# Optimization experiments

Hardware: AMD Instinct MI355X
Metric: run time of the kernel (lower is better)

## Reference

```python
import jax, jax.numpy as jnp
import numpy as np

B, Q, H, KVH, HD, HS = 2, 1024, 32, 8, 64, 2048
LCK = 2  # number of pre-existing cache entries
N_REP = H // KVH


def setup_inputs() -> dict:
    key = jax.random.key(0)
    ks = jax.random.split(key, 8)
    s = 0.02
    causal = jnp.tril(jnp.ones((Q, Q), dtype=bool))
    attention_mask = jnp.where(causal, 0.0, -1e9).astype(jnp.float32)[None, None]  # [1,1,Q,Q]
    return {
        "hidden_states": jax.random.normal(ks[0], (B, Q, 2 * HS), jnp.float32),
        "Wq": jax.random.normal(ks[1], (H * HD, 2 * HS), jnp.float32) * s,
        "Wk": jax.random.normal(ks[2], (KVH * HD, 2 * HS), jnp.float32) * s,
        "Wv": jax.random.normal(ks[3], (KVH * HD, 2 * HS), jnp.float32) * s,
        "Wo": jax.random.normal(ks[4], (H * HD, HS), jnp.float32).T * s,  # [HS, H*HD]
        "cache_k": jax.random.normal(ks[5], (LCK, B, H, Q, HD), jnp.float32),
        "cache_v": jax.random.normal(ks[6], (LCK, B, H, Q, HD), jnp.float32),
        "attention_mask": attention_mask,
        "position_ids": jnp.broadcast_to(jnp.arange(Q, dtype=jnp.int32), (B, Q)),
    }


def _rotate_half(x):
    return jnp.concatenate([-x[..., HD // 2:], x[..., :HD // 2]], axis=-1)


def reference(hidden_states, Wq, Wk, Wv, Wo, cache_k, cache_v, attention_mask, position_ids):
    b, q_len, _ = hidden_states.shape
    # QKV projections (Linear with weight [out,in]: x @ W.T)
    q = (hidden_states @ Wq.T).reshape(b, q_len, H, HD).transpose(0, 2, 1, 3)    # [b,H,q,hd]
    k = (hidden_states @ Wk.T).reshape(b, q_len, KVH, HD).transpose(0, 2, 1, 3)  # [b,KVH,q,hd]
    v = (hidden_states @ Wv.T).reshape(b, q_len, KVH, HD).transpose(0, 2, 1, 3)

    # RoPE at positions position_ids + lck (lck = LCK cached entries)
    inv_freq = 1.0 / (10000.0 ** (jnp.arange(0, HD, 2, dtype=jnp.float32) / HD))
    pos = (position_ids + LCK).astype(jnp.float32)                 # [b,q]
    freqs = pos[..., None] * inv_freq                              # [b,q,hd/2]
    emb = jnp.concatenate([freqs, freqs], axis=-1)                 # [b,q,hd]
    cos = jnp.cos(emb)[:, None]                                    # [b,1,q,hd]
    sin = jnp.sin(emb)[:, None]
    q = q * cos + _rotate_half(q) * sin
    k = k * cos + _rotate_half(k) * sin

    # GQA repeat_kv
    k = jnp.repeat(k, N_REP, axis=1)  # [b,H,q,hd]
    v = jnp.repeat(v, N_REP, axis=1)

    scale = 1.0 / np.sqrt(HD)
    k0, v0 = cache_k[0], cache_v[0]
    # full attention against first cache entry (+ causal mask)
    w0 = jnp.einsum('bhqd,bhkd->bhqk', q, k0) * scale + attention_mask  # [b,H,q,q]
    # per-step diagonal attention against remaining cache entries + fresh k
    tail_k = jnp.concatenate([cache_k[1:], k[None]], axis=0)  # [LCK,b,H,q,hd]
    tail_v = jnp.concatenate([cache_v[1:], v[None]], axis=0)
    wtail = jnp.einsum('bhqd,nbhqd->bhqn', q, tail_k) * scale  # [b,H,q,LCK]

    w = jnp.concatenate([w0, wtail], axis=-1)
    w = jax.nn.softmax(w.astype(jnp.float32), axis=-1).astype(q.dtype)

    out = jnp.einsum('bhqk,bhkd->bhqd', w[..., :q_len], v0)
    out = out + jnp.einsum('bhqn,nbhqd->bhqd', w[..., q_len:], tail_v)

    out = out.transpose(0, 2, 1, 3).reshape(b, q_len, H * HD)
    return out @ Wo.T  # [b,q,HS]
```

## Files before the change

kernel.cpp:

```cpp
#include <hip/hip_runtime.h>
#include <hip/hip_bf16.h>
#include <math.h>

#define B_    2
#define Q_    1024
#define H_    32
#define KVH_  8
#define HD_   64
#define HS_   2048
#define NREP_ 4
#define KIN_  (2*HS_)
#define M_    (B_*Q_)
#define QKVN_ (H_*HD_ + 2*KVH_*HD_)
#define AOW_  (H_*HD_)
#define SCALE_ 0.125f

typedef __attribute__((ext_vector_type(8))) short bf16x8;
typedef __attribute__((ext_vector_type(4))) float f32x4;
typedef unsigned short u16;

static __device__ __forceinline__ u16 f2b(float f) {
  union { float f; unsigned int u; } c; c.f = f;
  unsigned int r = (c.u + 0x7fffu + ((c.u >> 16) & 1u)) >> 16;
  return (u16)r;
}
static __device__ __forceinline__ float b2f(u16 s) {
  union { unsigned int u; float f; } c;
  c.u = ((unsigned int)s) << 16;
  return c.f;
}
static __device__ __forceinline__ unsigned long long pack4s(float4 v, float sc) {
  return (unsigned long long)f2b(v.x*sc) |
         ((unsigned long long)f2b(v.y*sc) << 16) |
         ((unsigned long long)f2b(v.z*sc) << 32) |
         ((unsigned long long)f2b(v.w*sc) << 48);
}

#define GLOAD(SRC, DST) __builtin_amdgcn_global_load_lds( \
    (const __attribute__((address_space(1))) void*)(SRC), \
    (__attribute__((address_space(3))) void*)(DST), 16, 0, 0)

__global__ __launch_bounds__(256) void cast_f32_bf16(
    const float* __restrict__ src, u16* __restrict__ dst, long n)
{
  long i = ((long)blockIdx.x * blockDim.x + threadIdx.x) * 8;
  if (i >= n) return;
  float4 a = *(const float4*)(src + i);
  float4 b = *(const float4*)(src + i + 4);
  unsigned long long o[2] = {pack4s(a, 1.f), pack4s(b, 1.f)};
  *(float4*)(dst + i) = *(const float4*)o;
}

__global__ __launch_bounds__(256) void cast_kv(
    const float* __restrict__ k0, const float* __restrict__ v0,
    u16* __restrict__ Kb, u16* __restrict__ Vtb)
{
  __shared__ float Vs[64][65];
  const int kt = blockIdx.x, bh = blockIdx.y;
  const int t = threadIdx.x;
  const int r = t >> 2, seg = t & 3;

  {
    const float* sp = k0 + ((size_t)bh*Q_ + (kt<<6) + r)*64;
    u16* dp = Kb + ((size_t)bh*Q_ + (kt<<6) + r)*64;
#pragma unroll
    for (int c2 = 2*seg; c2 < 2*seg+2; ++c2) {
      int ca = c2 ^ (r & 7);
      float4 a = *(const float4*)(sp + ca*8);
      float4 b = *(const float4*)(sp + ca*8 + 4);
      unsigned long long o[2] = {pack4s(a,1.f), pack4s(b,1.f)};
      *(float4*)(dp + c2*8) = *(const float4*)o;
    }
  }
  {
    const float* sp = v0 + ((size_t)bh*Q_ + (kt<<6) + r)*64 + seg*16;
#pragma unroll
    for (int c = 0; c < 4; ++c) {
      float4 v = *(const float4*)(sp + 4*c);
      Vs[r][seg*16 + 4*c + 0] = v.x; Vs[r][seg*16 + 4*c + 1] = v.y;
      Vs[r][seg*16 + 4*c + 2] = v.z; Vs[r][seg*16 + 4*c + 3] = v.w;
    }
  }
  __syncthreads();
  {
    const int d = r;
    u16* dp = Vtb + ((size_t)bh*64 + d)*Q_ + (kt<<6);
#pragma unroll
    for (int c2 = 2*seg; c2 < 2*seg+2; ++c2) {
      int ca = c2 ^ (d & 7);
      u16 o[8];
#pragma unroll
      for (int j = 0; j < 8; ++j) o[j] = f2b(Vs[ca*8 + j][d]);
      *(float4*)(dp + c2*8) = *(const float4*)o;
    }
  }
}

template<bool OUT_BF16>
__global__ __launch_bounds__(256, 3) void gemm_nt(
    const u16* __restrict__ A, const u16* __restrict__ W,
    void* __restrict__ Cv, int K, int ldc)
{
  __shared__ u16 As[2*128*64];
  __shared__ u16 Bs[2*64*64];
  const int m0 = blockIdx.y << 7, n0 = blockIdx.x << 6;
  const int t = threadIdx.x;
  const int wave = t >> 6, lane = t & 63;
  const int wr = wave >> 1, wc = wave & 1;

  f32x4 acc[4][2] = {};

  const int lrow8 = lane >> 3;
  const int lcsw  = ((lane & 7) ^ lrow8) * 8;
  const int fr    = lane & 15;
  const int g     = lane >> 4;

#define GEMM_STAGE(BUF, K0) do { \
    _Pragma("unroll") \
    for (int p = 0; p < 4; ++p) { \
      int rbase = p * 32 + wave * 8; \
      GLOAD(A + (size_t)(m0 + rbase + lrow8) * K + (K0) + lcsw, \
            As + (BUF)*8192 + rbase * 64); \
    } \
    _Pragma("unroll") \
    for (int p = 0; p < 2; ++p) { \
      int rbase = p * 32 + wave * 8; \
      GLOAD(W + (size_t)(n0 + rbase + lrow8) * K + (K0) + lcsw, \
            Bs + (BUF)*4096 + rbase * 64); \
    } \
  } while(0)

  GEMM_STAGE(0, 0);
  int cur = 0;
  for (int k0 = 0; k0 < K; k0 += 64) {
    if (k0 + 64 < K) {
      GEMM_STAGE(cur ^ 1, k0 + 64);
      asm volatile("s_waitcnt vmcnt(6)" ::: "memory");
    } else {
      asm volatile("s_waitcnt vmcnt(0)" ::: "memory");
    }
    asm volatile("s_barrier" ::: "memory");

    const u16* Ab = As + cur*8192;
    const u16* Bb = Bs + cur*4096;
    bf16x8 af[4][2], bfr[2][2];
#pragma unroll
    for (int kk = 0; kk < 2; ++kk) {
      int ck = kk * 4 + g;
#pragma unroll
      for (int mi = 0; mi < 4; ++mi) {
        int row = wr * 64 + mi * 16 + fr;
        af[mi][kk] = *(const bf16x8*)(Ab + row * 64 + ((ck ^ (row & 7)) << 3));
      }
#pragma unroll
      for (int ni = 0; ni < 2; ++ni) {
        int row = wc * 32 + ni * 16 + fr;
        bfr[ni][kk] = *(const bf16x8*)(Bb + row * 64 + ((ck ^ (row & 7)) << 3));
      }
    }
    __builtin_amdgcn_s_setprio(1);
#pragma unroll
    for (int kk = 0; kk < 2; ++kk)
#pragma unroll
      for (int mi = 0; mi < 4; ++mi)
#pragma unroll
        for (int ni = 0; ni < 2; ++ni)
          acc[mi][ni] = __builtin_amdgcn_mfma_f32_16x16x32_bf16(af[mi][kk], bfr[ni][kk], acc[mi][ni], 0, 0, 0);
    __builtin_amdgcn_s_setprio(0);
    asm volatile("s_barrier" ::: "memory");
    cur ^= 1;
  }
#undef GEMM_STAGE

#pragma unroll
  for (int mi = 0; mi < 4; ++mi) {
    int rbase = m0 + wr * 64 + mi * 16 + (lane >> 4) * 4;
#pragma unroll
    for (int ni = 0; ni < 2; ++ni) {
      int col = n0 + wc * 32 + ni * 16 + (lane & 15);
#pragma unroll
      for (int r = 0; r < 4; ++r) {
        if (OUT_BF16) ((u16*)Cv)[(size_t)(rbase + r) * ldc + col] = f2b(acc[mi][ni][r]);
        else          ((float*)Cv)[(size_t)(rbase + r) * ldc + col] = acc[mi][ni][r];
      }
    }
  }
}

__global__ void rope_kernel(u16* __restrict__ Yb, const int* __restrict__ pos_ids)
{
  int idx = blockIdx.x * blockDim.x + threadIdx.x;
  const int nwork = M_ * 40 * 4;
  if (idx >= nwork) return;
  int dblk = idx & 3;
  int hr   = idx >> 2;
  int head = hr % 40;
  int m    = hr / 40;
  u16* row = Yb + (size_t)m * QKVN_ + head * 64;
  int d0 = dblk * 8;
  float4 lo4 = *(const float4*)(row + d0);
  float4 hi4 = *(const float4*)(row + d0 + 32);
  const u16* lo = (const u16*)&lo4;
  const u16* hi = (const u16*)&hi4;
  float p = (float)(pos_ids[m] + 2);
  float qs = (head < 32) ? SCALE_ : 1.0f;
  u16 olo[8], ohi[8];
#pragma unroll
  for (int i = 0; i < 8; ++i) {
    int d = d0 + i;
    float inv = exp2f(-0.4152410118609203f * (float)d);
    float f = p * inv;
    float c, s;
    sincosf(f, &s, &c);
    float x0 = b2f(lo[i]), x1 = b2f(hi[i]);
    olo[i] = f2b((x0*c - x1*s) * qs);
    ohi[i] = f2b((x1*c + x0*s) * qs);
  }
  *(float4*)(row + d0)      = *(const float4*)olo;
  *(float4*)(row + d0 + 32) = *(const float4*)ohi;
}

__global__ __launch_bounds__(256, 3) void attn_mfma(
    const u16* __restrict__ Yb,
    const u16* __restrict__ Kb,
    const u16* __restrict__ Vtb,
    const float* __restrict__ cache_k,
    const float* __restrict__ cache_v,
    u16* __restrict__ AOb)
{
  __shared__ u16 Qs[64*64];
  __shared__ u16 Ps[64*64];
  __shared__ u16 Ks[2*64*64];
  __shared__ u16 Vt[2*64*64];

  const int bid = blockIdx.x;
  const int xcd = bid & 7, within = bid >> 3;
  const int w16 = within & 15;
  const int qt = (w16 & 1) ? (15 - (w16 >> 1)) : (w16 >> 1);
  const int pair = xcd * 8 + (within >> 4);
  const int h = pair >> 1, b = pair & 1;
  const int bh = b * H_ + h;

  const int t = threadIdx.x;
  const int wave = t >> 6, lane = t & 63;
  const int g = lane >> 4, sub = lane & 15;
  const int wq0 = wave * 16;
  const int srow = (lane >> 3);
  const int scc  = lane & 7;

  const u16* KbT = Kb + (size_t)bh * Q_ * 64;
  const u16* VtT = Vtb + (size_t)bh * 64 * Q_;

#define ATTN_STAGE(BUF, KT) do { \
    _Pragma("unroll") \
    for (int p = 0; p < 2; ++p) { \
      int r = p*32 + wave*8 + srow; \
      GLOAD(KbT + (size_t)(((KT)<<6) + r)*64 + scc*8, Ks + (BUF)*4096 + p*2048 + wave*512); \
      GLOAD(VtT + (size_t)r*Q_ + ((KT)<<6) + scc*8,   Vt + (BUF)*4096 + p*2048 + wave*512); \
    } \
  } while(0)

  {
#pragma unroll
    for (int p = 0; p < 2; ++p) {
      int r = p*32 + wave*8 + srow;
      GLOAD(Yb + (size_t)(b*Q_ + (qt<<6) + r)*QKVN_ + h*64 + ((scc ^ (r&7))<<3),
            Qs + p*2048 + wave*512);
    }
  }
  ATTN_STAGE(0, 0);
  asm volatile("s_waitcnt vmcnt(4)" ::: "memory");
  asm volatile("s_barrier" ::: "memory");

  bf16x8 qb[2];
#pragma unroll
  for (int kk = 0; kk < 2; ++kk) {
    int row = wq0 + sub;
    qb[kk] = *(const bf16x8*)&Qs[row*64 + (((4*kk+g) ^ (row&7))<<3)];
  }

  float m_run = -3e38f, l_run = 0.f;
  f32x4 acc_o[4] = {};
  int cur = 0;

  for (int kt = 0; kt <= qt; ++kt) {
    if (kt < qt) {
      ATTN_STAGE(cur ^ 1, kt + 1);
      asm volatile("s_waitcnt vmcnt(4)" ::: "memory");
    } else {
      asm volatile("s_waitcnt vmcnt(0)" ::: "memory");
    }
    asm volatile("s_barrier" ::: "memory");

    const u16* ksb = Ks + cur*4096;
    const u16* vtb = Vt + cur*4096;

    f32x4 s[4] = {};
    __builtin_amdgcn_s_setprio(1);
#pragma unroll
    for (int kk = 0; kk < 2; ++kk) {
      int kb = 4*kk + g;
#pragma unroll
      for (int cb = 0; cb < 4; ++cb) {
        int krow = cb*16 + sub;
        bf16x8 kf = *(const bf16x8*)&ksb[krow*64 + ((kb ^ (krow&7))<<3)];
        s[cb] = __builtin_amdgcn_mfma_f32_16x16x32_bf16(kf, qb[kk], s[cb], 0, 0, 0);
      }
    }
    __builtin_amdgcn_s_setprio(0);

    if (kt == qt) {
#pragma unroll
      for (int cb = 0; cb < 4; ++cb)
#pragma unroll
        for (int r = 0; r < 4; ++r)
          if (cb*16 + 4*g + r > wq0 + sub) s[cb][r] = -3e38f;
    }

    float mt = -3e38f;
#pragma unroll
    for (int cb = 0; cb < 4; ++cb)
#pragma unroll
      for (int r = 0; r < 4; ++r) mt = fmaxf(mt, s[cb][r]);
    mt = fmaxf(mt, __shfl_xor(mt, 16, 64));
    mt = fmaxf(mt, __shfl_xor(mt, 32, 64));

    float al = 1.0f;
    if (__any(mt > m_run + 8.f)) {
      float mnew = fmaxf(m_run, mt);
      al = __expf(m_run - mnew);
      m_run = mnew;
      int base = (lane & 48) + ((lane & 48) >> 2);
#pragma unroll
      for (int r = 0; r < 4; ++r) {
        float alr = __shfl(al, base + r, 64);
#pragma unroll
        for (int db = 0; db < 4; ++db) acc_o[db][r] *= alr;
      }
    }

    float sum = 0.f;
#pragma unroll
    for (int cb = 0; cb < 4; ++cb) {
      float p0 = __expf(s[cb][0]-m_run), p1 = __expf(s[cb][1]-m_run);
      float p2 = __expf(s[cb][2]-m_run), p3 = __expf(s[cb][3]-m_run);
      sum += (p0+p1)+(p2+p3);
      unsigned long long pk =
          (unsigned long long)((unsigned int)f2b(p0) | ((unsigned int)f2b(p1)<<16)) |
          ((unsigned long long)((unsigned int)f2b(p2) | ((unsigned int)f2b(p3)<<16)) << 32);
      int col8 = cb*2 + (g>>1);
      int dst = (wq0 + sub)*64 + ((col8 ^ (sub&7))<<3) + ((g&1)<<2);
      *(unsigned long long*)&Ps[dst] = pk;
    }
    sum += __shfl_xor(sum, 16, 64);
    sum += __shfl_xor(sum, 32, 64);
    l_run = l_run*al + sum;

    __builtin_amdgcn_s_setprio(1);
#pragma unroll
    for (int kk = 0; kk < 2; ++kk) {
      bf16x8 pa = *(const bf16x8*)&Ps[(wq0 + sub)*64 + (((4*kk+g) ^ (sub&7))<<3)];
#pragma unroll
      for (int db = 0; db < 4; ++db) {
        int drow = db*16 + sub;
        bf16x8 vf = *(const bf16x8*)&vtb[drow*64 + (((4*kk+g) ^ (drow&7))<<3)];
        acc_o[db] = __builtin_amdgcn_mfma_f32_16x16x32_bf16(pa, vf, acc_o[db], 0, 0, 0);
      }
    }
    __builtin_amdgcn_s_setprio(0);
    asm volatile("s_barrier" ::: "memory");
    cur ^= 1;
  }
#undef ATTN_STAGE

  const int qrow_mine = wq0 + sub;
  const int qpos_mine = (qt<<6) + qrow_mine;
  float e1 = 0.f, e2 = 0.f;
  {
    const float* k1p = cache_k + ((size_t)((B_ + b)*H_ + h)*Q_ + qpos_mine)*HD_ + g*16;
    const u16*   kfp = Yb + (size_t)(b*Q_ + qpos_mine)*QKVN_ + H_*HD_ + (h/NREP_)*HD_ + g*16;
    float qv[16];
#pragma unroll
    for (int half = 0; half < 2; ++half) {
      int kb = 2*g + half;
      bf16x8 qq = *(const bf16x8*)&Qs[qrow_mine*64 + ((kb ^ (qrow_mine&7))<<3)];
#pragma unroll
      for (int i = 0; i < 8; ++i) qv[half*8 + i] = b2f(((u16)qq[i]));
    }
    float4 kf4a = *(const float4*)kfp;
    float4 kf4b = *(const float4*)(kfp + 8);
    const u16* kf16a = (const u16*)&kf4a;
    const u16* kf16b = (const u16*)&kf4b;
#pragma unroll
    for (int c = 0; c < 4; ++c) {
      float4 kv1 = *(const float4*)(k1p + 4*c);
      e1 += qv[4*c]*kv1.x + qv[4*c+1]*kv1.y + qv[4*c+2]*kv1.z + qv[4*c+3]*kv1.w;
    }
#pragma unroll
    for (int i = 0; i < 8; ++i) {
      e2 += qv[i]   * b2f(kf16a[i]);
      e2 += qv[8+i] * b2f(kf16b[i]);
    }
  }
  e1 += __shfl_xor(e1, 16, 64); e1 += __shfl_xor(e1, 32, 64);
  e2 += __shfl_xor(e2, 16, 64); e2 += __shfl_xor(e2, 32, 64);

#pragma unroll
  for (int r = 0; r < 4; ++r) {
    int row = 4*g + r;
    int src = (lane & 48) | row;
    float e1r = __shfl(e1, src, 64);
    float e2r = __shfl(e2, src, 64);
    float m_r = __shfl(m_run, src, 64);
    float l_r = __shfl(l_run, src, 64);
    float mnew = fmaxf(m_r, fmaxf(e1r, e2r));
    float alr = __expf(m_r - mnew);
    float w1  = __expf(e1r - mnew);
    float w2  = __expf(e2r - mnew);
    float linv = 1.f / (l_r*alr + w1 + w2);
    int qpos = (qt<<6) + wq0 + row;
    const float* v1p = cache_v + ((size_t)((B_ + b)*H_ + h)*Q_ + qpos)*HD_;
    const u16*   vfp = Yb + (size_t)(b*Q_ + qpos)*QKVN_ + (H_*HD_ + KVH_*HD_) + (h/NREP_)*HD_;
    u16* op = AOb + (size_t)(b*Q_ + qpos)*AOW_ + h*HD_;
#pragma unroll
    for (int db = 0; db < 4; ++db) {
      int d = db*16 + sub;
      float o = (acc_o[db][r]*alr + w1*v1p[d] + w2*b2f(vfp[d])) * linv;
      op[d] = f2b(o);
    }
  }
}

extern "C" void kernel_launch(void* const* d_in, const int* in_sizes, int n_in,
                              void* d_out, int out_size, void* d_ws, size_t ws_size,
                              hipStream_t stream) {
  const float* hidden  = (const float*)d_in[0];
  const float* Wq      = (const float*)d_in[1];
  const float* Wk      = (const float*)d_in[2];
  const float* Wv      = (const float*)d_in[3];
  const float* Wo      = (const float*)d_in[4];
  const float* cache_k = (const float*)d_in[5];
  const float* cache_v = (const float*)d_in[6];
  const int*   pos_ids = (const int*)d_in[8];
  float* out = (float*)d_out;

  char* ws = (char*)d_ws;
  u16* Yb  = (u16*)ws;  ws += (size_t)M_ * QKVN_ * 2;
  u16* Xb  = (u16*)ws;  ws += (size_t)M_ * KIN_ * 2;
  u16* Wb  = (u16*)ws;  ws += (size_t)QKVN_ * KIN_ * 2;
  u16* Wob = (u16*)ws;  ws += (size_t)HS_ * AOW_ * 2;
  u16* Kb  = (u16*)ws;  ws += (size_t)B_*H_*Q_*64 * 2;
  u16* Vtb = (u16*)ws;  ws += (size_t)B_*H_*Q_*64 * 2;
  u16* AOb = Xb;

  {
    long n;
    n = (long)M_ * KIN_;
    cast_f32_bf16<<<dim3((n/8 + 255)/256), 256, 0, stream>>>(hidden, Xb, n);
    n = (long)H_*HD_*KIN_;
    cast_f32_bf16<<<dim3((n/8 + 255)/256), 256, 0, stream>>>(Wq, Wb, n);
    n = (long)KVH_*HD_*KIN_;
    cast_f32_bf16<<<dim3((n/8 + 255)/256), 256, 0, stream>>>(Wk, Wb + (size_t)2048*KIN_, n);
    cast_f32_bf16<<<dim3((n/8 + 255)/256), 256, 0, stream>>>(Wv, Wb + (size_t)2560*KIN_, n);
    n = (long)HS_ * AOW_;
    cast_f32_bf16<<<dim3((n/8 + 255)/256), 256, 0, stream>>>(Wo, Wob, n);
  }
  cast_kv<<<dim3(16, 64), 256, 0, stream>>>(cache_k, cache_v, Kb, Vtb);

  gemm_nt<true><<<dim3(QKVN_/64, M_/128), 256, 0, stream>>>(Xb, Wb, (void*)Yb, KIN_, QKVN_);
  rope_kernel<<<dim3((M_*40*4 + 255)/256), 256, 0, stream>>>(Yb, pos_ids);
  attn_mfma<<<dim3(1024), 256, 0, stream>>>(Yb, Kb, Vtb, cache_k, cache_v, AOb);
  gemm_nt<false><<<dim3(HS_/64, M_/128), 256, 0, stream>>>(AOb, Wob, (void*)out, AOW_, HS_);
}
```

Before: 180.7 us.

## Fuse casts into one kernel, fold RoPE into QKV GEMM, widen attention blocks

The five weight and activation cast launches are merged into a single grid-stride kernel. RoPE and the Q scaling move into the QKV GEMM epilogue, with partner halves exchanged through shared memory, so the separate rope pass over Yb goes away. Attention blocks grow to 512 threads covering 128 query rows that share each K/V tile load, and per-wave causal skipping is added. This trades launch overhead and repeated K/V traffic for higher register and LDS pressure per block and extra syncs in the GEMM epilogue.

```diff
diff --git a/kernel.cpp b/kernel.cpp
--- a/kernel.cpp
+++ b/kernel.cpp
@@ -40,15 +40,29 @@
     (const __attribute__((address_space(1))) void*)(SRC), \
     (__attribute__((address_space(3))) void*)(DST), 16, 0, 0)
 
-__global__ __launch_bounds__(256) void cast_f32_bf16(
-    const float* __restrict__ src, u16* __restrict__ dst, long n)
+__global__ __launch_bounds__(256) void cast_all(
+    const float* __restrict__ hidden, const float* __restrict__ Wq,
+    const float* __restrict__ Wk, const float* __restrict__ Wv,
+    const float* __restrict__ Wo,
+    u16* __restrict__ Xb, u16* __restrict__ Wb, u16* __restrict__ Wob)
 {
-  long i = ((long)blockIdx.x * blockDim.x + threadIdx.x) * 8;
-  if (i >= n) return;
-  float4 a = *(const float4*)(src + i);
-  float4 b = *(const float4*)(src + i + 4);
-  unsigned long long o[2] = {pack4s(a, 1.f), pack4s(b, 1.f)};
-  *(float4*)(dst + i) = *(const float4*)o;
+  const int U0 = 1048576;
+  const int U1 = U0 + 1048576;
+  const int U2 = U1 + 262144;
+  const int U3 = U2 + 262144;
+  const int U4 = U3 + 524288;
+  for (int u = blockIdx.x*blockDim.x + threadIdx.x; u < U4; u += gridDim.x*blockDim.x) {
+    const float* src; u16* dst;
+    if (u < U0)      { src = hidden + (size_t)u*8;   dst = Xb + (size_t)u*8; }
+    else if (u < U1) { src = Wq + (size_t)(u-U0)*8;  dst = Wb + (size_t)(u-U0)*8; }
+    else if (u < U2) { src = Wk + (size_t)(u-U1)*8;  dst = Wb + (size_t)2048*KIN_ + (size_t)(u-U1)*8; }
+    else if (u < U3) { src = Wv + (size_t)(u-U2)*8;  dst = Wb + (size_t)2560*KIN_ + (size_t)(u-U2)*8; }
+    else             { src = Wo + (size_t)(u-U3)*8;  dst = Wob + (size_t)(u-U3)*8; }
+    float4 a = *(const float4*)src;
+    float4 bb = *(const float4*)(src + 4);
+    unsigned long long o[2] = {pack4s(a, 1.f), pack4s(bb, 1.f)};
+    *(float4*)dst = *(const float4*)o;
+  }
 }
 
 __global__ __launch_bounds__(256) void cast_kv(
@@ -59,7 +73,6 @@
   const int kt = blockIdx.x, bh = blockIdx.y;
   const int t = threadIdx.x;
   const int r = t >> 2, seg = t & 3;
-
   {
     const float* sp = k0 + ((size_t)bh*Q_ + (kt<<6) + r)*64;
     u16* dp = Kb + ((size_t)bh*Q_ + (kt<<6) + r)*64;
@@ -96,10 +109,10 @@
   }
 }
 
-template<bool OUT_BF16>
+template<bool QKV>
 __global__ __launch_bounds__(256, 3) void gemm_nt(
     const u16* __restrict__ A, const u16* __restrict__ W,
-    void* __restrict__ Cv, int K, int ldc)
+    void* __restrict__ Cv, int K, int ldc, const int* __restrict__ pos_ids)
 {
   __shared__ u16 As[2*128*64];
   __shared__ u16 Bs[2*64*64];
@@ -172,55 +185,59 @@
   }
 #undef GEMM_STAGE
 
-#pragma unroll
-  for (int mi = 0; mi < 4; ++mi) {
-    int rbase = m0 + wr * 64 + mi * 16 + (lane >> 4) * 4;
-#pragma unroll
-    for (int ni = 0; ni < 2; ++ni) {
-      int col = n0 + wc * 32 + ni * 16 + (lane & 15);
+  if (QKV && n0 < 2560) {
+    float* xch = (float*)As;
+    __syncthreads();
+#pragma unroll
+    for (int mi = 0; mi < 4; ++mi)
+#pragma unroll
+      for (int ni = 0; ni < 2; ++ni)
+#pragma unroll
+        for (int r = 0; r < 4; ++r)
+          xch[(wr*64 + mi*16 + g*4 + r)*64 + wc*32 + ni*16 + (lane & 15)] = acc[mi][ni][r];
+    __syncthreads();
+    const bool isq = (n0 < 2048);
+    u16* outp = (u16*)Cv;
+#pragma unroll
+    for (int mi = 0; mi < 4; ++mi) {
 #pragma unroll
       for (int r = 0; r < 4; ++r) {
-        if (OUT_BF16) ((u16*)Cv)[(size_t)(rbase + r) * ldc + col] = f2b(acc[mi][ni][r]);
-        else          ((float*)Cv)[(size_t)(rbase + r) * ldc + col] = acc[mi][ni][r];
-      }
-    }
-  }
-}
-
-__global__ void rope_kernel(u16* __restrict__ Yb, const int* __restrict__ pos_ids)
-{
-  int idx = blockIdx.x * blockDim.x + threadIdx.x;
-  const int nwork = M_ * 40 * 4;
-  if (idx >= nwork) return;
-  int dblk = idx & 3;
-  int hr   = idx >> 2;
-  int head = hr % 40;
-  int m    = hr / 40;
-  u16* row = Yb + (size_t)m * QKVN_ + head * 64;
-  int d0 = dblk * 8;
-  float4 lo4 = *(const float4*)(row + d0);
-  float4 hi4 = *(const float4*)(row + d0 + 32);
-  const u16* lo = (const u16*)&lo4;
-  const u16* hi = (const u16*)&hi4;
-  float p = (float)(pos_ids[m] + 2);
-  float qs = (head < 32) ? SCALE_ : 1.0f;
-  u16 olo[8], ohi[8];
-#pragma unroll
-  for (int i = 0; i < 8; ++i) {
-    int d = d0 + i;
-    float inv = exp2f(-0.4152410118609203f * (float)d);
-    float f = p * inv;
-    float c, s;
-    sincosf(f, &s, &c);
-    float x0 = b2f(lo[i]), x1 = b2f(hi[i]);
-    olo[i] = f2b((x0*c - x1*s) * qs);
-    ohi[i] = f2b((x1*c + x0*s) * qs);
-  }
-  *(float4*)(row + d0)      = *(const float4*)olo;
-  *(float4*)(row + d0 + 32) = *(const float4*)ohi;
-}
-
-__global__ __launch_bounds__(256, 3) void attn_mfma(
+        int rl = wr*64 + mi*16 + g*4 + r;
+        int m = m0 + rl;
+        float p = (float)(pos_ids[m] + 2);
+#pragma unroll
+        for (int ni = 0; ni < 2; ++ni) {
+          int dr = ni*16 + (lane & 15);
+          float inv = exp2f(-0.4152410118609203f * (float)dr);
+          float f = p * inv;
+          float c, s;
+          sincosf(f, &s, &c);
+          float mine = acc[mi][ni][r];
+          float part = xch[rl*64 + ((wc^1)*32 + ni*16 + (lane & 15))];
+          float outv = (wc == 0) ? (mine*c - part*s) : (mine*c + part*s);
+          if (isq) outv *= SCALE_;
+          outp[(size_t)m * ldc + n0 + wc*32 + ni*16 + (lane & 15)] = f2b(outv);
+        }
+      }
+    }
+  } else {
+#pragma unroll
+    for (int mi = 0; mi < 4; ++mi) {
+      int rbase = m0 + wr * 64 + mi * 16 + g * 4;
+#pragma unroll
+      for (int ni = 0; ni < 2; ++ni) {
+        int col = n0 + wc * 32 + ni * 16 + (lane & 15);
+#pragma unroll
+        for (int r = 0; r < 4; ++r) {
+          if (QKV) ((u16*)Cv)[(size_t)(rbase + r) * ldc + col] = f2b(acc[mi][ni][r]);
+          else     ((float*)Cv)[(size_t)(rbase + r) * ldc + col] = acc[mi][ni][r];
+        }
+      }
+    }
+  }
+}
+
+__global__ __launch_bounds__(512, 4) void attn_mfma(
     const u16* __restrict__ Yb,
     const u16* __restrict__ Kb,
     const u16* __restrict__ Vtb,
@@ -228,16 +245,16 @@
     const float* __restrict__ cache_v,
     u16* __restrict__ AOb)
 {
-  __shared__ u16 Qs[64*64];
-  __shared__ u16 Ps[64*64];
+  __shared__ u16 Qs[128*64];
+  __shared__ u16 Ps[128*64];
   __shared__ u16 Ks[2*64*64];
   __shared__ u16 Vt[2*64*64];
 
   const int bid = blockIdx.x;
   const int xcd = bid & 7, within = bid >> 3;
-  const int w16 = within & 15;
-  const int qt = (w16 & 1) ? (15 - (w16 >> 1)) : (w16 >> 1);
-  const int pair = xcd * 8 + (within >> 4);
+  const int w8 = within & 7;
+  const int qtb = (w8 & 1) ? (7 - (w8 >> 1)) : (w8 >> 1);
+  const int pair = xcd * 8 + (within >> 3);
   const int h = pair >> 1, b = pair & 1;
   const int bh = b * H_ + h;
 
@@ -245,31 +262,28 @@
   const int wave = t >> 6, lane = t & 63;
   const int g = lane >> 4, sub = lane & 15;
   const int wq0 = wave * 16;
-  const int srow = (lane >> 3);
+  const int srow = lane >> 3;
   const int scc  = lane & 7;
 
   const u16* KbT = Kb + (size_t)bh * Q_ * 64;
   const u16* VtT = Vtb + (size_t)bh * 64 * Q_;
 
 #define ATTN_STAGE(BUF, KT) do { \
-    _Pragma("unroll") \
-    for (int p = 0; p < 2; ++p) { \
-      int r = p*32 + wave*8 + srow; \
-      GLOAD(KbT + (size_t)(((KT)<<6) + r)*64 + scc*8, Ks + (BUF)*4096 + p*2048 + wave*512); \
-      GLOAD(VtT + (size_t)r*Q_ + ((KT)<<6) + scc*8,   Vt + (BUF)*4096 + p*2048 + wave*512); \
-    } \
+    int r_ = wave*8 + srow; \
+    GLOAD(KbT + (size_t)(((KT)<<6) + r_)*64 + scc*8, Ks + (BUF)*4096 + wave*512); \
+    GLOAD(VtT + (size_t)r_*Q_ + ((KT)<<6) + scc*8,   Vt + (BUF)*4096 + wave*512); \
   } while(0)
 
   {
 #pragma unroll
     for (int p = 0; p < 2; ++p) {
-      int r = p*32 + wave*8 + srow;
-      GLOAD(Yb + (size_t)(b*Q_ + (qt<<6) + r)*QKVN_ + h*64 + ((scc ^ (r&7))<<3),
-            Qs + p*2048 + wave*512);
+      int r = p*64 + wave*8 + srow;
+      GLOAD(Yb + (size_t)(b*Q_ + qtb*128 + r)*QKVN_ + h*64 + ((scc ^ (r&7))<<3),
+            Qs + p*4096 + wave*512);
     }
   }
   ATTN_STAGE(0, 0);
-  asm volatile("s_waitcnt vmcnt(4)" ::: "memory");
+  asm volatile("s_waitcnt vmcnt(2)" ::: "memory");
   asm volatile("s_barrier" ::: "memory");
 
   bf16x8 qb[2];
@@ -282,99 +296,102 @@
   float m_run = -3e38f, l_run = 0.f;
   f32x4 acc_o[4] = {};
   int cur = 0;
-
-  for (int kt = 0; kt <= qt; ++kt) {
-    if (kt < qt) {
+  const int nkt = 2*qtb + 2;
+
+  for (int kt = 0; kt < nkt; ++kt) {
+    if (kt + 1 < nkt) {
       ATTN_STAGE(cur ^ 1, kt + 1);
-      asm volatile("s_waitcnt vmcnt(4)" ::: "memory");
+      asm volatile("s_waitcnt vmcnt(2)" ::: "memory");
     } else {
       asm volatile("s_waitcnt vmcnt(0)" ::: "memory");
     }
     asm volatile("s_barrier" ::: "memory");
 
-    const u16* ksb = Ks + cur*4096;
-    const u16* vtb = Vt + cur*4096;
-
-    f32x4 s[4] = {};
-    __builtin_amdgcn_s_setprio(1);
-#pragma unroll
-    for (int kk = 0; kk < 2; ++kk) {
-      int kb = 4*kk + g;
+    if (kt*64 <= qtb*128 + wq0 + 15) {
+      const u16* ksb = Ks + cur*4096;
+      const u16* vtb = Vt + cur*4096;
+
+      f32x4 s[4] = {};
+      __builtin_amdgcn_s_setprio(1);
+#pragma unroll
+      for (int kk = 0; kk < 2; ++kk) {
+        int kb = 4*kk + g;
+#pragma unroll
+        for (int cb = 0; cb < 4; ++cb) {
+          int krow = cb*16 + sub;
+          bf16x8 kf = *(const bf16x8*)&ksb[krow*64 + ((kb ^ (krow&7))<<3)];
+          s[cb] = __builtin_amdgcn_mfma_f32_16x16x32_bf16(kf, qb[kk], s[cb], 0, 0, 0);
+        }
+      }
+      __builtin_amdgcn_s_setprio(0);
+
+      if (kt >= 2*qtb) {
+#pragma unroll
+        for (int cb = 0; cb < 4; ++cb)
+#pragma unroll
+          for (int r = 0; r < 4; ++r)
+            if (kt*64 + cb*16 + 4*g + r > qtb*128 + wq0 + sub) s[cb][r] = -3e38f;
+      }
+
+      float mt = -3e38f;
+#pragma unroll
+      for (int cb = 0; cb < 4; ++cb)
+#pragma unroll
+        for (int r = 0; r < 4; ++r) mt = fmaxf(mt, s[cb][r]);
+      mt = fmaxf(mt, __shfl_xor(mt, 16, 64));
+      mt = fmaxf(mt, __shfl_xor(mt, 32, 64));
+
+      float al = 1.0f;
+      if (__any(mt > m_run + 8.f)) {
+        float mnew = fmaxf(m_run, mt);
+        al = __expf(m_run - mnew);
+        m_run = mnew;
+        int base = (lane & 48) + ((lane & 48) >> 2);
+#pragma unroll
+        for (int r = 0; r < 4; ++r) {
+          float alr = __shfl(al, base + r, 64);
+#pragma unroll
+          for (int db = 0; db < 4; ++db) acc_o[db][r] *= alr;
+        }
+      }
+
+      float sum = 0.f;
 #pragma unroll
       for (int cb = 0; cb < 4; ++cb) {
-        int krow = cb*16 + sub;
-        bf16x8 kf = *(const bf16x8*)&ksb[krow*64 + ((kb ^ (krow&7))<<3)];
-        s[cb] = __builtin_amdgcn_mfma_f32_16x16x32_bf16(kf, qb[kk], s[cb], 0, 0, 0);
-      }
-    }
-    __builtin_amdgcn_s_setprio(0);
-
-    if (kt == qt) {
-#pragma unroll
-      for (int cb = 0; cb < 4; ++cb)
-#pragma unroll
-        for (int r = 0; r < 4; ++r)
-          if (cb*16 + 4*g + r > wq0 + sub) s[cb][r] = -3e38f;
-    }
-
-    float mt = -3e38f;
-#pragma unroll
-    for (int cb = 0; cb < 4; ++cb)
-#pragma unroll
-      for (int r = 0; r < 4; ++r) mt = fmaxf(mt, s[cb][r]);
-    mt = fmaxf(mt, __shfl_xor(mt, 16, 64));
-    mt = fmaxf(mt, __shfl_xor(mt, 32, 64));
-
-    float al = 1.0f;
-    if (__any(mt > m_run + 8.f)) {
-      float mnew = fmaxf(m_run, mt);
-      al = __expf(m_run - mnew);
-      m_run = mnew;
-      int base = (lane & 48) + ((lane & 48) >> 2);
-#pragma unroll
-      for (int r = 0; r < 4; ++r) {
-        float alr = __shfl(al, base + r, 64);
-#pragma unroll
-        for (int db = 0; db < 4; ++db) acc_o[db][r] *= alr;
-      }
-    }
-
-    float sum = 0.f;
-#pragma unroll
-    for (int cb = 0; cb < 4; ++cb) {
-      float p0 = __expf(s[cb][0]-m_run), p1 = __expf(s[cb][1]-m_run);
-      float p2 = __expf(s[cb][2]-m_run), p3 = __expf(s[cb][3]-m_run);
-      sum += (p0+p1)+(p2+p3);
-      unsigned long long pk =
-          (unsigned long long)((unsigned int)f2b(p0) | ((unsigned int)f2b(p1)<<16)) |
-          ((unsigned long long)((unsigned int)f2b(p2) | ((unsigned int)f2b(p3)<<16)) << 32);
-      int col8 = cb*2 + (g>>1);
-      int dst = (wq0 + sub)*64 + ((col8 ^ (sub&7))<<3) + ((g&1)<<2);
-      *(unsigned long long*)&Ps[dst] = pk;
-    }
-    sum += __shfl_xor(sum, 16, 64);
-    sum += __shfl_xor(sum, 32, 64);
-    l_run = l_run*al + sum;
-
-    __builtin_amdgcn_s_setprio(1);
-#pragma unroll
-    for (int kk = 0; kk < 2; ++kk) {
-      bf16x8 pa = *(const bf16x8*)&Ps[(wq0 + sub)*64 + (((4*kk+g) ^ (sub&7))<<3)];
-#pragma unroll
-      for (int db = 0; db < 4; ++db) {
-        int drow = db*16 + sub;
-        bf16x8 vf = *(const bf16x8*)&vtb[drow*64 + (((4*kk+g) ^ (drow&7))<<3)];
-        acc_o[db] = __builtin_amdgcn_mfma_f32_16x16x32_bf16(pa, vf, acc_o[db], 0, 0, 0);
-      }
-    }
-    __builtin_amdgcn_s_setprio(0);
+        float p0 = __expf(s[cb][0]-m_run), p1 = __expf(s[cb][1]-m_run);
+        float p2 = __expf(s[cb][2]-m_run), p3 = __expf(s[cb][3]-m_run);
+        sum += (p0+p1)+(p2+p3);
+        unsigned long long pk =
+            (unsigned long long)((unsigned int)f2b(p0) | ((unsigned int)f2b(p1)<<16)) |
+            ((unsigned long long)((unsigned int)f2b(p2) | ((unsigned int)f2b(p3)<<16)) << 32);
+        int col8 = cb*2 + (g>>1);
+        int dst = (wq0 + sub)*64 + ((col8 ^ (sub&7))<<3) + ((g&1)<<2);
+        *(unsigned long long*)&Ps[dst] = pk;
+      }
+      sum += __shfl_xor(sum, 16, 64);
+      sum += __shfl_xor(sum, 32, 64);
+      l_run = l_run*al + sum;
+
+      __builtin_amdgcn_s_setprio(1);
+#pragma unroll
+      for (int kk = 0; kk < 2; ++kk) {
+        bf16x8 pa = *(const bf16x8*)&Ps[(wq0 + sub)*64 + (((4*kk+g) ^ (sub&7))<<3)];
+#pragma unroll
+        for (int db = 0; db < 4; ++db) {
+          int drow = db*16 + sub;
+          bf16x8 vf = *(const bf16x8*)&vtb[drow*64 + (((4*kk+g) ^ (drow&7))<<3)];
+          acc_o[db] = __builtin_amdgcn_mfma_f32_16x16x32_bf16(pa, vf, acc_o[db], 0, 0, 0);
+        }
+      }
+      __builtin_amdgcn_s_setprio(0);
+    }
     asm volatile("s_barrier" ::: "memory");
     cur ^= 1;
   }
 #undef ATTN_STAGE
 
   const int qrow_mine = wq0 + sub;
-  const int qpos_mine = (qt<<6) + qrow_mine;
+  const int qpos_mine = qtb*128 + qrow_mine;
   float e1 = 0.f, e2 = 0.f;
   {
     const float* k1p = cache_k + ((size_t)((B_ + b)*H_ + h)*Q_ + qpos_mine)*HD_ + g*16;
@@ -418,7 +435,7 @@
     float w1  = __expf(e1r - mnew);
     float w2  = __expf(e2r - mnew);
     float linv = 1.f / (l_r*alr + w1 + w2);
-    int qpos = (qt<<6) + wq0 + row;
+    int qpos = qtb*128 + wq0 + row;
     const float* v1p = cache_v + ((size_t)((B_ + b)*H_ + h)*Q_ + qpos)*HD_;
     const u16*   vfp = Yb + (size_t)(b*Q_ + qpos)*QKVN_ + (H_*HD_ + KVH_*HD_) + (h/NREP_)*HD_;
     u16* op = AOb + (size_t)(b*Q_ + qpos)*AOW_ + h*HD_;
@@ -453,22 +470,10 @@
   u16* Vtb = (u16*)ws;  ws += (size_t)B_*H_*Q_*64 * 2;
   u16* AOb = Xb;
 
-  {
-    long n;
-    n = (long)M_ * KIN_;
-    cast_f32_bf16<<<dim3((n/8 + 255)/256), 256, 0, stream>>>(hidden, Xb, n);
-    n = (long)H_*HD_*KIN_;
-    cast_f32_bf16<<<dim3((n/8 + 255)/256), 256, 0, stream>>>(Wq, Wb, n);
-    n = (long)KVH_*HD_*KIN_;
-    cast_f32_bf16<<<dim3((n/8 + 255)/256), 256, 0, stream>>>(Wk, Wb + (size_t)2048*KIN_, n);
-    cast_f32_bf16<<<dim3((n/8 + 255)/256), 256, 0, stream>>>(Wv, Wb + (size_t)2560*KIN_, n);
-    n = (long)HS_ * AOW_;
-    cast_f32_bf16<<<dim3((n/8 + 255)/256), 256, 0, stream>>>(Wo, Wob, n);
-  }
+  cast_all<<<dim3(2048), 256, 0, stream>>>(hidden, Wq, Wk, Wv, Wo, Xb, Wb, Wob);
   cast_kv<<<dim3(16, 64), 256, 0, stream>>>(cache_k, cache_v, Kb, Vtb);
 
-  gemm_nt<true><<<dim3(QKVN_/64, M_/128), 256, 0, stream>>>(Xb, Wb, (void*)Yb, KIN_, QKVN_);
-  rope_kernel<<<dim3((M_*40*4 + 255)/256), 256, 0, stream>>>(Yb, pos_ids);
-  attn_mfma<<<dim3(1024), 256, 0, stream>>>(Yb, Kb, Vtb, cache_k, cache_v, AOb);
-  gemm_nt<false><<<dim3(HS_/64, M_/128), 256, 0, stream>>>(AOb, Wob, (void*)out, AOW_, HS_);
-}
+  gemm_nt<true><<<dim3(QKVN_/64, M_/128), 256, 0, stream>>>(Xb, Wb, (void*)Yb, KIN_, QKVN_, pos_ids);
+  attn_mfma<<<dim3(512), 512, 0, stream>>>(Yb, Kb, Vtb, cache_k, cache_v, AOb);
+  gemm_nt<false><<<dim3(HS_/64, M_/128), 256, 0, stream>>>(AOb, Wob, (void*)out, AOW_, HS_, nullptr);
+}
```

Result: faster. 168.3 us (-6.9%).
